# Kernel tuning notes

Hardware: AMD Instinct MI355X
Metric: run time of the kernel (lower is better)

## Reference

```python
import jax, jax.numpy as jnp
import numpy as np

N_EMBD = 1024
N_HEAD = 16


def setup_inputs() -> dict:
    key = jax.random.key(0)
    k1, k2, k3, k4, k5 = jax.random.split(key, 5)
    B, T, C = 4, 2048, N_EMBD
    s = 1.0 / np.sqrt(C)
    x = jax.random.normal(k1, (B, T, C), dtype=jnp.float32)
    w_weight = jax.random.normal(k2, (3 * C, C), dtype=jnp.float32) * s
    w_bias = jax.random.normal(k3, (3 * C,), dtype=jnp.float32) * s
    proj_weight = jax.random.normal(k4, (C, C), dtype=jnp.float32) * s
    proj_bias = jax.random.normal(k5, (C,), dtype=jnp.float32) * s
    return {"x": x, "w_weight": w_weight, "w_bias": w_bias,
            "proj_weight": proj_weight, "proj_bias": proj_bias}


def reference(x, w_weight, w_bias, proj_weight, proj_bias):
    B, T, C = x.shape
    nh = N_HEAD
    hs = C // nh
    # fused QKV projection (torch Linear: x @ W^T + b)
    wei = jnp.einsum('btc,oc->bto', x, w_weight) + w_bias
    k, q, v = jnp.split(wei, 3, axis=-1)  # note: chunk order is k, q, v
    # [B, T, nh, hs] -> [B, nh, T, hs]
    key_ = k.reshape(B, T, nh, hs).transpose(0, 2, 1, 3)
    query = q.reshape(B, T, nh, hs).transpose(0, 2, 1, 3)
    value = v.reshape(B, T, nh, hs).transpose(0, 2, 1, 3)
    scale = hs ** (-0.5)
    weight = jnp.einsum('bhqd,bhkd->bhqk', query, key_) * scale
    weight = jax.nn.softmax(weight, axis=-1)
    out = jnp.einsum('bhqk,bhkd->bhqd', weight, value)  # [B, nh, T, hs]
    # Faithful to source bug: transpose(1,2) is discarded; view is taken on
    # the (B, nh, T, hs) layout directly.
    out = out.reshape(B, T, C)
    out = jnp.einsum('btc,oc->bto', out, proj_weight) + proj_bias
    return out
```

## Files before the change

kernel.cpp:

```cpp
#include <hip/hip_runtime.h>
#include <hip/hip_bf16.h>


typedef __attribute__((ext_vector_type(8)))  short bf16x8;
typedef __attribute__((ext_vector_type(4)))  float f32x4;
typedef __attribute__((ext_vector_type(16))) float f32x16;
typedef __attribute__((ext_vector_type(2)))  unsigned u32x2;

typedef __attribute__((address_space(3))) unsigned lds_u32_t;
typedef __attribute__((address_space(1))) unsigned glb_u32_t;

__device__ __forceinline__ void async_cp16(const short* g, short* l) {
    __builtin_amdgcn_global_load_lds((glb_u32_t*)g, (lds_u32_t*)l, 16, 0, 0);
}

__device__ __forceinline__ float exp2fast(float x) {
    return __builtin_amdgcn_exp2f(x);
}

__device__ __forceinline__ short f2bf(float f) {
    union { float f; unsigned u; } v; v.f = f;
    unsigned r = v.u + 0x7fffu + ((v.u >> 16) & 1u);
    return (short)(r >> 16);
}

__device__ __forceinline__ unsigned cvt_pk_bf16(float lo, float hi) {
    unsigned r;
    asm("v_cvt_pk_bf16_f32 %0, %1, %2" : "=v"(r) : "v"(lo), "v"(hi));
    return r;
}

__global__ __launch_bounds__(256) void cvt_kernel(const float4* __restrict__ in,
                                                  short4* __restrict__ out, int n4) {
    int i = blockIdx.x * 256 + threadIdx.x;
    if (i < n4) {
        float4 v = in[i];
        short4 o;
        o.x = f2bf(v.x); o.y = f2bf(v.y); o.z = f2bf(v.z); o.w = f2bf(v.w);
        out[i] = o;
    }
}

template<int EPI>
__global__ __launch_bounds__(256) void gemm_bf16(
    const short* __restrict__ A, const short* __restrict__ W,
    const float* __restrict__ bias, float* __restrict__ outF,
    short* __restrict__ kout, short* __restrict__ qout, short* __restrict__ vtout,
    int M, int N, int K)
{
    __shared__ short lA[2][128 * 64];
    __shared__ short lB[2][128 * 64];
    const int tid  = threadIdx.x;
    const int lane = tid & 63;
    const int wave = tid >> 6;
    const int wM = (wave >> 1) * 64;
    const int wN = (wave & 1) * 64;
    const int l15 = lane & 15, l4 = lane >> 4;
    const int rsw = (lane & 7) << 3;
    const int rowBase = blockIdx.y * 128;
    const int colBase = blockIdx.x * 128;

    auto STAGE = [&](int t, int buf) {
        const int k0 = t * 64;
        #pragma unroll
        for (int i = 0; i < 4; ++i) {
            int idx = i * 256 + tid;
            int r   = idx >> 3;
            int cp  = ((idx & 7) ^ (r & 7)) * 8;
            int eo  = idx * 8;
            async_cp16(A + (size_t)(rowBase + r) * K + k0 + cp, &lA[buf][eo]);
            async_cp16(W + (size_t)(colBase + r) * K + k0 + cp, &lB[buf][eo]);
        }
    };

    f32x4 acc[4][4] = {};
    const int NT = K >> 6;

    STAGE(0, 0);
    __syncthreads();

    int cur = 0;
    for (int t = 0; t < NT; ++t) {
        if (t + 1 < NT) STAGE(t + 1, cur ^ 1);
        #pragma unroll
        for (int kt = 0; kt < 2; ++kt) {
            bf16x8 af[4], bfr[4];
            #pragma unroll
            for (int mt = 0; mt < 4; ++mt)
                af[mt] = *(const bf16x8*)(
                    &lA[cur][(wM + mt * 16 + l15) * 64 + ((kt * 32 + l4 * 8) ^ rsw)]);
            #pragma unroll
            for (int nt = 0; nt < 4; ++nt)
                bfr[nt] = *(const bf16x8*)(
                    &lB[cur][(wN + nt * 16 + l15) * 64 + ((kt * 32 + l4 * 8) ^ rsw)]);
            #pragma unroll
            for (int mt = 0; mt < 4; ++mt)
                #pragma unroll
                for (int nt = 0; nt < 4; ++nt)
                    acc[mt][nt] = __builtin_amdgcn_mfma_f32_16x16x32_bf16(
                        af[mt], bfr[nt], acc[mt][nt], 0, 0, 0);
        }
        __syncthreads();
        cur ^= 1;
    }

    #pragma unroll
    for (int mt = 0; mt < 4; ++mt) {
        #pragma unroll
        for (int nt = 0; nt < 4; ++nt) {
            const int n  = colBase + wN + nt * 16 + l15;
            const int mb = rowBase + wM + mt * 16 + l4 * 4;
            const float bv = bias[n];
            #pragma unroll
            for (int r = 0; r < 4; ++r) {
                const int m = mb + r;
                float val = acc[mt][nt][r] + bv;
                if (EPI == 0) {
                    int b = m >> 11, t = m & 2047;
                    int j = n >> 10, hd = n & 1023;
                    int h = hd >> 6, d = hd & 63;
                    size_t base = ((size_t)(b * 16 + h) * 2048 + t) * 64 + d;
                    if (j == 0)      kout[base] = f2bf(val);
                    else if (j == 1) qout[base] = f2bf(val * 0.180336879f);
                    else             vtout[((size_t)(b * 16 + h) * 64 + d) * 2048 + t] = f2bf(val);
                } else {
                    outF[(size_t)m * N + n] = val;
                }
            }
        }
    }
}

__global__ __launch_bounds__(256) void attn_kernel(
    const short* __restrict__ Q, const short* __restrict__ Km,
    const short* __restrict__ Vt, short* __restrict__ O)
{
    __shared__ short kbuf[2][64 * 64];
    __shared__ short vbuf[2][64 * 64];

    const int tid  = threadIdx.x;
    const int lane = tid & 63;
    const int wave = tid >> 6;
    const int l31 = lane & 31;
    const int l1  = lane >> 5;

    const int b     = blockIdx.x;
    const int xcd   = b & 7;
    const int inner = b >> 3;
    const int bx    = inner & 15;
    const int bh    = xcd * 8 + (inner >> 4);
    const int q0    = bx * 128 + wave * 32;

    const short* Qh = Q  + (size_t)bh * 2048 * 64;
    const short* Kh = Km + (size_t)bh * 2048 * 64;
    const short* Vh = Vt + (size_t)bh * 64 * 2048;

    const int i8 = lane >> 3, i7 = lane & 7;
    const int srcCol = 8 * (i7 ^ i8);
    const int rsw    = (l31 & 7) << 3;

    const short* src[4];
    short* dst0[4];
    int step;
    if (wave < 2) {
        #pragma unroll
        for (int c = 0; c < 4; ++c) {
            int j = wave * 4 + c;
            src[c]  = Kh + (size_t)(8 * j + i8) * 64 + srcCol;
            dst0[c] = &kbuf[0][j * 512 + lane * 8];
        }
        step = 64 * 64;
    } else {
        #pragma unroll
        for (int c = 0; c < 4; ++c) {
            int j = (wave - 2) * 4 + c;
            src[c]  = Vh + (size_t)(8 * j + i8) * 2048 + srcCol;
            dst0[c] = &vbuf[0][j * 512 + lane * 8];
        }
        step = 64;
    }
    auto STAGE = [&](int buf) {
        #pragma unroll
        for (int c = 0; c < 4; ++c) {
            async_cp16(src[c], dst0[c] + buf * 4096);
            src[c] += step;
        }
    };

    bf16x8 qf[4];
    #pragma unroll
    for (int s = 0; s < 4; ++s)
        qf[s] = *(const bf16x8*)(Qh + (size_t)(q0 + l31) * 64 + s * 16 + l1 * 8);

    union { unsigned u[4]; bf16x8 v; } onesu;
    #pragma unroll
    for (int j = 0; j < 4; ++j) onesu.u[j] = 0x3F803F80u;
    const bf16x8 onesf = onesu.v;

    f32x16 o[2] = {};
    f32x16 ol   = {};

    STAGE(0);
    __syncthreads();

    int cur = 0;
    for (int it = 0; it < 32; ++it) {
        if (it < 31) STAGE(cur ^ 1);

        f32x16 s2[2] = {};
        __builtin_amdgcn_s_setprio(1);
        #pragma unroll
        for (int t = 0; t < 2; ++t) {
            #pragma unroll
            for (int s = 0; s < 4; ++s) {
                bf16x8 kf = *(const bf16x8*)(
                    &kbuf[cur][(t * 32 + l31) * 64 + ((s * 16 + l1 * 8) ^ rsw)]);
                s2[t] = __builtin_amdgcn_mfma_f32_32x32x16_bf16(kf, qf[s], s2[t], 0, 0, 0);
            }
        }
        __builtin_amdgcn_s_setprio(0);

        #pragma unroll
        for (int t = 0; t < 2; ++t)
            #pragma unroll
            for (int i = 0; i < 16; ++i)
                s2[t][i] = exp2fast(s2[t][i]);

        bf16x8 pa[4];
        #pragma unroll
        for (int t = 0; t < 2; ++t) {
            #pragma unroll
            for (int sl = 0; sl < 2; ++sl) {
                unsigned A0 = cvt_pk_bf16(s2[t][8 * sl + 0], s2[t][8 * sl + 1]);
                unsigned A1 = cvt_pk_bf16(s2[t][8 * sl + 2], s2[t][8 * sl + 3]);
                unsigned B0 = cvt_pk_bf16(s2[t][8 * sl + 4], s2[t][8 * sl + 5]);
                unsigned B1 = cvt_pk_bf16(s2[t][8 * sl + 6], s2[t][8 * sl + 7]);
                u32x2 ra = __builtin_amdgcn_permlane32_swap(A0, B0, false, false);
                u32x2 rb = __builtin_amdgcn_permlane32_swap(A1, B1, false, false);
                union { unsigned u[4]; bf16x8 v; } w;
                w.u[0] = ra.x;
                w.u[1] = rb.x;
                w.u[2] = ra.y;
                w.u[3] = rb.y;
                pa[2 * t + sl] = w.v;
            }
        }

        __builtin_amdgcn_s_setprio(1);
        #pragma unroll
        for (int s = 0; s < 4; ++s) {
            #pragma unroll
            for (int dt = 0; dt < 2; ++dt) {
                bf16x8 vf = *(const bf16x8*)(
                    &vbuf[cur][(dt * 32 + l31) * 64 + ((s * 16 + l1 * 8) ^ rsw)]);
                o[dt] = __builtin_amdgcn_mfma_f32_32x32x16_bf16(pa[s], vf, o[dt], 0, 0, 0);
            }
            ol = __builtin_amdgcn_mfma_f32_32x32x16_bf16(pa[s], onesf, ol, 0, 0, 0);
        }
        __builtin_amdgcn_s_setprio(0);

        __syncthreads();
        cur ^= 1;
    }

    #pragma unroll
    for (int g = 0; g < 4; ++g)
        #pragma unroll
        for (int rr = 0; rr < 4; ++rr) {
            float invl = 1.f / ol[g * 4 + rr];
            int qrow = q0 + rr + 8 * g + 4 * l1;
            size_t base = ((size_t)bh * 2048 + qrow) * 64 + l31;
            O[base]      = f2bf(o[0][g * 4 + rr] * invl);
            O[base + 32] = f2bf(o[1][g * 4 + rr] * invl);
        }
}

extern "C" void kernel_launch(void* const* d_in, const int* in_sizes, int n_in,
                              void* d_out, int out_size, void* d_ws, size_t ws_size,
                              hipStream_t stream) {
    const float* x  = (const float*)d_in[0];
    const float* ww = (const float*)d_in[1];
    const float* wb = (const float*)d_in[2];
    const float* pwt = (const float*)d_in[3];
    const float* pb  = (const float*)d_in[4];
    float* out = (float*)d_out;

    short* ws  = (short*)d_ws;
    short* xb  = ws;
    short* wwb = xb  + 8192 * 1024;
    short* pwb = wwb + 3072 * 1024;
    short* qb  = pwb + 1024 * 1024;
    short* kb  = qb  + 64 * 2048 * 64;
    short* vtb = kb  + 64 * 2048 * 64;
    short* ob  = vtb + 64 * 2048 * 64;

    cvt_kernel<<<2097152 / 256, 256, 0, stream>>>((const float4*)x,  (short4*)xb,  2097152);
    cvt_kernel<<< 786432 / 256, 256, 0, stream>>>((const float4*)ww, (short4*)wwb,  786432);
    cvt_kernel<<< 262144 / 256, 256, 0, stream>>>((const float4*)pwt,(short4*)pwb,  262144);

    gemm_bf16<0><<<dim3(24, 64), 256, 0, stream>>>(
        xb, wwb, wb, nullptr, kb, qb, vtb, 8192, 3072, 1024);

    attn_kernel<<<1024, 256, 0, stream>>>(qb, kb, vtb, ob);

    gemm_bf16<1><<<dim3(8, 64), 256, 0, stream>>>(
        ob, pwb, pb, out, nullptr, nullptr, nullptr, 8192, 1024, 1024);
}
```

Before: 219.0 us.

## Deepen GEMM pipeline to four K32 slots and merge conversion kernels

The three fp32-to-bf16 conversion launches become one kernel that picks its source tensor by block index, which removes two launches. The bf16 GEMM now stages K in 32-wide slices across a four-slot LDS ring, prefetching two slices ahead. It waits with explicit vmcnt counters and a single s_barrier per slice instead of a full __syncthreads. This aims to hide global load latency better, at the cost of a new swizzle and finer-grained barriers that risk races or bank conflicts.

Measured after the change: 240.5 us. 1.1x slower.

```diff
diff --git a/kernel.cpp b/kernel.cpp
--- a/kernel.cpp
+++ b/kernel.cpp
@@ -30,15 +30,19 @@
     return r;
 }
 
-__global__ __launch_bounds__(256) void cvt_kernel(const float4* __restrict__ in,
-                                                  short4* __restrict__ out, int n4) {
-    int i = blockIdx.x * 256 + threadIdx.x;
-    if (i < n4) {
-        float4 v = in[i];
-        short4 o;
-        o.x = f2bf(v.x); o.y = f2bf(v.y); o.z = f2bf(v.z); o.w = f2bf(v.w);
-        out[i] = o;
-    }
+__global__ __launch_bounds__(256) void cvt3_kernel(
+    const float4* __restrict__ x,  const float4* __restrict__ ww,
+    const float4* __restrict__ pw, short4* __restrict__ xb,
+    short4* __restrict__ wwb,      short4* __restrict__ pwb) {
+    const int b = blockIdx.x;
+    const float4* in; short4* out; int i;
+    if (b < 8192)       { in = x;  out = xb;  i = b * 256 + threadIdx.x; }
+    else if (b < 11264) { in = ww; out = wwb; i = (b - 8192) * 256 + threadIdx.x; }
+    else                { in = pw; out = pwb; i = (b - 11264) * 256 + threadIdx.x; }
+    float4 v = in[i];
+    short4 o;
+    o.x = f2bf(v.x); o.y = f2bf(v.y); o.z = f2bf(v.z); o.w = f2bf(v.w);
+    out[i] = o;
 }
 
 template<int EPI>
@@ -48,61 +52,66 @@
     short* __restrict__ kout, short* __restrict__ qout, short* __restrict__ vtout,
     int M, int N, int K)
 {
-    __shared__ short lA[2][128 * 64];
-    __shared__ short lB[2][128 * 64];
+    __shared__ short lA[4][128 * 32];
+    __shared__ short lB[4][128 * 32];
     const int tid  = threadIdx.x;
     const int lane = tid & 63;
     const int wave = tid >> 6;
     const int wM = (wave >> 1) * 64;
     const int wN = (wave & 1) * 64;
     const int l15 = lane & 15, l4 = lane >> 4;
-    const int rsw = (lane & 7) << 3;
+    const int rsw = (l15 & 3) << 3;
     const int rowBase = blockIdx.y * 128;
     const int colBase = blockIdx.x * 128;
 
-    auto STAGE = [&](int t, int buf) {
-        const int k0 = t * 64;
-        #pragma unroll
-        for (int i = 0; i < 4; ++i) {
+    auto STAGE = [&](int t, int slot) {
+        const int k0 = t * 32;
+        #pragma unroll
+        for (int i = 0; i < 2; ++i) {
             int idx = i * 256 + tid;
-            int r   = idx >> 3;
-            int cp  = ((idx & 7) ^ (r & 7)) * 8;
-            int eo  = idx * 8;
-            async_cp16(A + (size_t)(rowBase + r) * K + k0 + cp, &lA[buf][eo]);
-            async_cp16(W + (size_t)(colBase + r) * K + k0 + cp, &lB[buf][eo]);
+            int r   = idx >> 2;
+            int cp  = ((idx & 3) ^ (r & 3)) * 8;
+            async_cp16(A + (size_t)(rowBase + r) * K + k0 + cp, &lA[slot][idx * 8]);
+            async_cp16(W + (size_t)(colBase + r) * K + k0 + cp, &lB[slot][idx * 8]);
         }
     };
 
     f32x4 acc[4][4] = {};
-    const int NT = K >> 6;
+
+    auto COMPUTE = [&](int slot) {
+        bf16x8 af[4], bfr[4];
+        const int co = l4 * 8;
+        #pragma unroll
+        for (int mt = 0; mt < 4; ++mt)
+            af[mt] = *(const bf16x8*)(&lA[slot][(wM + mt * 16 + l15) * 32 + (co ^ rsw)]);
+        #pragma unroll
+        for (int nt = 0; nt < 4; ++nt)
+            bfr[nt] = *(const bf16x8*)(&lB[slot][(wN + nt * 16 + l15) * 32 + (co ^ rsw)]);
+        #pragma unroll
+        for (int mt = 0; mt < 4; ++mt)
+            #pragma unroll
+            for (int nt = 0; nt < 4; ++nt)
+                acc[mt][nt] = __builtin_amdgcn_mfma_f32_16x16x32_bf16(
+                    af[mt], bfr[nt], acc[mt][nt], 0, 0, 0);
+    };
+
+    const int NT = K >> 5;
 
     STAGE(0, 0);
-    __syncthreads();
-
-    int cur = 0;
-    for (int t = 0; t < NT; ++t) {
-        if (t + 1 < NT) STAGE(t + 1, cur ^ 1);
-        #pragma unroll
-        for (int kt = 0; kt < 2; ++kt) {
-            bf16x8 af[4], bfr[4];
-            #pragma unroll
-            for (int mt = 0; mt < 4; ++mt)
-                af[mt] = *(const bf16x8*)(
-                    &lA[cur][(wM + mt * 16 + l15) * 64 + ((kt * 32 + l4 * 8) ^ rsw)]);
-            #pragma unroll
-            for (int nt = 0; nt < 4; ++nt)
-                bfr[nt] = *(const bf16x8*)(
-                    &lB[cur][(wN + nt * 16 + l15) * 64 + ((kt * 32 + l4 * 8) ^ rsw)]);
-            #pragma unroll
-            for (int mt = 0; mt < 4; ++mt)
-                #pragma unroll
-                for (int nt = 0; nt < 4; ++nt)
-                    acc[mt][nt] = __builtin_amdgcn_mfma_f32_16x16x32_bf16(
-                        af[mt], bfr[nt], acc[mt][nt], 0, 0, 0);
-        }
-        __syncthreads();
-        cur ^= 1;
+    STAGE(1, 1);
+    asm volatile("s_waitcnt vmcnt(4)" ::: "memory");
+    asm volatile("s_barrier" ::: "memory");
+
+    for (int t = 0; t < NT - 2; ++t) {
+        STAGE(t + 2, (t + 2) & 3);
+        COMPUTE(t & 3);
+        asm volatile("s_waitcnt vmcnt(4)" ::: "memory");
+        asm volatile("s_barrier" ::: "memory");
     }
+    COMPUTE((NT - 2) & 3);
+    asm volatile("s_waitcnt vmcnt(0)" ::: "memory");
+    asm volatile("s_barrier" ::: "memory");
+    COMPUTE((NT - 1) & 3);
 
     #pragma unroll
     for (int mt = 0; mt < 4; ++mt) {
@@ -294,9 +303,9 @@
     short* vtb = kb  + 64 * 2048 * 64;
     short* ob  = vtb + 64 * 2048 * 64;
 
-    cvt_kernel<<<2097152 / 256, 256, 0, stream>>>((const float4*)x,  (short4*)xb,  2097152);
-    cvt_kernel<<< 786432 / 256, 256, 0, stream>>>((const float4*)ww, (short4*)wwb,  786432);
-    cvt_kernel<<< 262144 / 256, 256, 0, stream>>>((const float4*)pwt,(short4*)pwb,  262144);
+    cvt3_kernel<<<12288, 256, 0, stream>>>(
+        (const float4*)x, (const float4*)ww, (const float4*)pwt,
+        (short4*)xb, (short4*)wwb, (short4*)pwb);
 
     gemm_bf16<0><<<dim3(24, 64), 256, 0, stream>>>(
         xb, wwb, wb, nullptr, kb, qb, vtb, 8192, 3072, 1024);
```
